# Kernel tuning notes

Measured on AMD Instinct MI355X. Metric: run time of the kernel, lower is better.

Reference implementation:

```python
import jax, jax.numpy as jnp
import numpy as np


def setup_inputs() -> dict:
    key = jax.random.key(0)
    ks = jax.random.split(key, 5)
    B, T, I, H = 32, 2048, 512, 512
    scale = 1.0 / np.sqrt(H)
    return {
        "x": jax.random.normal(ks[0], (B, T, I), dtype=jnp.float32),
        "h_0": jnp.zeros((B, H), dtype=jnp.float32),
        "Wx": jax.random.normal(ks[1], (H, I), dtype=jnp.float32) * scale,
        "bx": jax.random.normal(ks[2], (H,), dtype=jnp.float32) * scale,
        "Wh": jax.random.normal(ks[3], (H, H), dtype=jnp.float32) * scale,
        "bh": jax.random.normal(ks[4], (H,), dtype=jnp.float32) * scale,
    }


def reference(x, h_0, Wx, bx, Wh, bh):
    # Precompute input projection for all timesteps in one big GEMM: [B,T,H]
    x_proj = jnp.einsum("bti,hi->bth", x, Wx) + bx + bh

    def step(h, xp_t):  # h: [B,H], xp_t: [B,H]
        h_new = jnp.tanh(xp_t + h @ Wh.T)
        return h_new, h_new

    # scan over time axis: move T to leading dim
    h_last, outs = jax.lax.scan(step, h_0, jnp.swapaxes(x_proj, 0, 1))
    outputs = jnp.swapaxes(outs, 0, 1)  # [B,T,H]
    return outputs, h_last
```

## Files before the change

kernel.cpp:

```cpp
#include <hip/hip_runtime.h>


constexpr int Bb = 32, Tt = 2048, Ii = 512, Hh = 512;
constexpr int NP = 8;
constexpr int RP = Hh / NP;

static __device__ __forceinline__ float fast_tanh(float x) {
    float ax = fabsf(x);
    float e = __expf(-2.0f * ax);
    float r = (1.0f - e) / (1.0f + e);
    return copysignf(r, x);
}

__global__ __launch_bounds__(256, 2)
void xproj_gemm(const float* __restrict__ x, const float* __restrict__ Wx,
                const float* __restrict__ bx, const float* __restrict__ bh,
                float* __restrict__ xp)
{
    constexpr int BM = 128, BK = 16, LDT = BM + 4;
    __shared__ float As[BK][LDT];
    __shared__ float Bs[BK][LDT];

    const int tid = threadIdx.x;
    const int m0 = blockIdx.x * BM;
    const int n0 = blockIdx.y * BM;
    const int lrow = tid >> 1;
    const int lkh  = (tid & 1) * 8;
    const int tx = tid & 15, ty = tid >> 4;

    float acc[2][2][4][4] = {};

    for (int k0 = 0; k0 < Ii; k0 += BK) {
        float4 a0 = *reinterpret_cast<const float4*>(&x[(size_t)(m0 + lrow) * Ii + k0 + lkh]);
        float4 a1 = *reinterpret_cast<const float4*>(&x[(size_t)(m0 + lrow) * Ii + k0 + lkh + 4]);
        float4 b0 = *reinterpret_cast<const float4*>(&Wx[(size_t)(n0 + lrow) * Ii + k0 + lkh]);
        float4 b1 = *reinterpret_cast<const float4*>(&Wx[(size_t)(n0 + lrow) * Ii + k0 + lkh + 4]);
        __syncthreads();
        As[lkh + 0][lrow] = a0.x; As[lkh + 1][lrow] = a0.y;
        As[lkh + 2][lrow] = a0.z; As[lkh + 3][lrow] = a0.w;
        As[lkh + 4][lrow] = a1.x; As[lkh + 5][lrow] = a1.y;
        As[lkh + 6][lrow] = a1.z; As[lkh + 7][lrow] = a1.w;
        Bs[lkh + 0][lrow] = b0.x; Bs[lkh + 1][lrow] = b0.y;
        Bs[lkh + 2][lrow] = b0.z; Bs[lkh + 3][lrow] = b0.w;
        Bs[lkh + 4][lrow] = b1.x; Bs[lkh + 5][lrow] = b1.y;
        Bs[lkh + 6][lrow] = b1.z; Bs[lkh + 7][lrow] = b1.w;
        __syncthreads();
        #pragma unroll
        for (int k = 0; k < BK; ++k) {
            float4 av[2], bv[2];
            av[0] = *reinterpret_cast<const float4*>(&As[k][ty * 4]);
            av[1] = *reinterpret_cast<const float4*>(&As[k][64 + ty * 4]);
            bv[0] = *reinterpret_cast<const float4*>(&Bs[k][tx * 4]);
            bv[1] = *reinterpret_cast<const float4*>(&Bs[k][64 + tx * 4]);
            #pragma unroll
            for (int rh = 0; rh < 2; ++rh) {
                const float* ap = reinterpret_cast<const float*>(&av[rh]);
                #pragma unroll
                for (int ch = 0; ch < 2; ++ch) {
                    const float* bp = reinterpret_cast<const float*>(&bv[ch]);
                    #pragma unroll
                    for (int i = 0; i < 4; ++i)
                        #pragma unroll
                        for (int j = 0; j < 4; ++j)
                            acc[rh][ch][i][j] += ap[i] * bp[j];
                }
            }
        }
    }

    float4 bias[2];
    #pragma unroll
    for (int ch = 0; ch < 2; ++ch) {
        int cb = n0 + ch * 64 + tx * 4;
        bias[ch] = make_float4(bx[cb] + bh[cb], bx[cb + 1] + bh[cb + 1],
                               bx[cb + 2] + bh[cb + 2], bx[cb + 3] + bh[cb + 3]);
    }
    #pragma unroll
    for (int rh = 0; rh < 2; ++rh)
        #pragma unroll
        for (int i = 0; i < 4; ++i) {
            size_t row = (size_t)(m0 + rh * 64 + ty * 4 + i);
            #pragma unroll
            for (int ch = 0; ch < 2; ++ch) {
                const float* bp = reinterpret_cast<const float*>(&bias[ch]);
                float4 v = make_float4(acc[rh][ch][i][0] + bp[0], acc[rh][ch][i][1] + bp[1],
                                       acc[rh][ch][i][2] + bp[2], acc[rh][ch][i][3] + bp[3]);
                *reinterpret_cast<float4*>(&xp[row * Hh + n0 + ch * 64 + tx * 4]) = v;
            }
        }
}

__global__ void zero_xbuf(unsigned long long* __restrict__ xb)
{
    xb[(size_t)blockIdx.x * 512 + threadIdx.x] = 0ull;
}

__global__ __launch_bounds__(512, 1)
void rnn_scan_mb(const float* __restrict__ Wh, const float* __restrict__ h0,
                 float* __restrict__ out, unsigned long long* __restrict__ xbuf)
{
    const int bid = blockIdx.x;
    const int c = bid & 31;
    const int P = bid >> 5;
    const int tid = threadIdx.x;
    const int w = tid >> 6;
    const int lane = tid & 63;
    const int hf = lane >> 5, lp = lane & 31;
    const int lrow0 = w * 8 + hf * 4;

    __shared__ __align__(16) float hs[Hh];
    __shared__ __align__(16) float pacc[RP][36];

    float4 wreg[4][4];
    #pragma unroll
    for (int s = 0; s < 4; ++s)
        #pragma unroll
        for (int q = 0; q < 4; ++q) {
            const float* ap = &Wh[(size_t)(P * RP + lrow0 + s) * Hh + q * 128 + lp * 4];
            asm volatile("global_load_dwordx4 %0, %1, off"
                         : "=v"(wreg[s][q]) : "v"(ap));
        }
    asm volatile("s_waitcnt vmcnt(0)" ::: "memory");

    hs[tid] = h0[(size_t)c * Hh + tid];

    float* ob = out + (size_t)c * Tt * Hh;
    unsigned long long* xb = xbuf + (size_t)c * 2 * Hh;

    float xp_cur = 0.f;
    if (w == P) xp_cur = ob[P * RP + lane];
    __syncthreads();

    for (int t = 0; t < Tt; ++t) {
        float4 hv[4];
        #pragma unroll
        for (int q = 0; q < 4; ++q)
            hv[q] = *reinterpret_cast<const float4*>(&hs[q * 128 + lp * 4]);
        #pragma unroll
        for (int s = 0; s < 4; ++s) {
            float sum = 0.f;
            #pragma unroll
            for (int q = 0; q < 4; ++q) {
                const float* wq = reinterpret_cast<const float*>(&wreg[s][q]);
                const float* hq = reinterpret_cast<const float*>(&hv[q]);
                sum += wq[0] * hq[0]; sum += wq[1] * hq[1];
                sum += wq[2] * hq[2]; sum += wq[3] * hq[3];
            }
            pacc[lrow0 + s][lp] = sum;
        }
        __syncthreads();

        if (w == P) {
            float ssum = xp_cur;
            #pragma unroll
            for (int q = 0; q < 8; ++q) {
                float4 p4 = *reinterpret_cast<const float4*>(&pacc[lane][q * 4]);
                ssum += (p4.x + p4.y) + (p4.z + p4.w);
            }
            float hval = fast_tanh(ssum);
            ob[(size_t)t * Hh + P * RP + lane] = hval;
            if (t + 1 < Tt) {
                unsigned long long msg =
                    ((unsigned long long)(unsigned)(t + 1) << 32) |
                    (unsigned long long)__float_as_uint(hval);
                __hip_atomic_store(&xb[(size_t)(t & 1) * Hh + P * RP + lane], msg,
                                   __ATOMIC_RELAXED, __HIP_MEMORY_SCOPE_AGENT);
                hs[P * RP + lane] = hval;
                xp_cur = ob[(size_t)(t + 1) * Hh + P * RP + lane];
            } else {
                out[(size_t)Bb * Tt * Hh + (size_t)c * Hh + P * RP + lane] = hval;
            }
        } else if (t + 1 < Tt) {
            const unsigned want = (unsigned)(t + 1);
            unsigned long long msg;
            do {
                msg = __hip_atomic_load(&xb[(size_t)(t & 1) * Hh + w * RP + lane],
                                        __ATOMIC_RELAXED, __HIP_MEMORY_SCOPE_AGENT);
            } while ((unsigned)(msg >> 32) != want);
            hs[w * RP + lane] = __uint_as_float((unsigned)msg);
        }
        __syncthreads();
    }
}

__global__ __launch_bounds__(512)
void rnn_scan_sb(const float* __restrict__ W, const float* __restrict__ h0,
                 float* __restrict__ out)
{
    const int b = blockIdx.x;
    const int j = threadIdx.x;
    __shared__ float hsb[2][Hh];
    hsb[0][j] = h0[(size_t)b * Hh + j];
    __syncthreads();

    float* ob = out + (size_t)b * Tt * Hh;
    const float* wbase = W + (size_t)j * Hh;

    float xp_cur = ob[j];
    int cur = 0;
    for (int t = 0; t < Tt; ++t) {
        float xp_next = (t + 1 < Tt) ? ob[(size_t)(t + 1) * Hh + j] : 0.0f;
        float4 a = make_float4(xp_cur, 0.0f, 0.0f, 0.0f);
        const float* h = hsb[cur];
        #pragma unroll 8
        for (int c4 = 0; c4 < Hh / 4; ++c4) {
            float4 wv = *reinterpret_cast<const float4*>(&wbase[c4 * 4]);
            float4 hv = *reinterpret_cast<const float4*>(&h[c4 * 4]);
            a.x += wv.x * hv.x; a.y += wv.y * hv.y;
            a.z += wv.z * hv.z; a.w += wv.w * hv.w;
        }
        float hn = tanhf((a.x + a.y) + (a.z + a.w));
        hsb[cur ^ 1][j] = hn;
        ob[(size_t)t * Hh + j] = hn;
        xp_cur = xp_next;
        cur ^= 1;
        __syncthreads();
    }
    out[(size_t)Bb * Tt * Hh + (size_t)b * Hh + j] = hsb[cur][j];
}

extern "C" void kernel_launch(void* const* d_in, const int* in_sizes, int n_in,
                              void* d_out, int out_size, void* d_ws, size_t ws_size,
                              hipStream_t stream)
{
    const float* x  = (const float*)d_in[0];
    const float* h0 = (const float*)d_in[1];
    const float* Wx = (const float*)d_in[2];
    const float* bx = (const float*)d_in[3];
    const float* Wh = (const float*)d_in[4];
    const float* bh = (const float*)d_in[5];
    float* out = (float*)d_out;

    dim3 g1(Bb * Tt / 128, Hh / 128);
    xproj_gemm<<<g1, 256, 0, stream>>>(x, Wx, bx, bh, out);

    const size_t xb_bytes = (size_t)Bb * 2 * Hh * sizeof(unsigned long long);
    if (ws_size >= xb_bytes) {
        unsigned long long* xbuf = (unsigned long long*)d_ws;
        zero_xbuf<<<64, 512, 0, stream>>>(xbuf);
        void* args[] = {(void*)&Wh, (void*)&h0, (void*)&out, (void*)&xbuf};
        hipLaunchCooperativeKernel((void*)rnn_scan_mb, dim3(NP * Bb), dim3(512),
                                   args, 0, stream);
    } else {
        rnn_scan_sb<<<Bb, Hh, 0, stream>>>(Wh, h0, out);
    }
}
```

Baseline: 3.012 ms.

## Overlap cross-block flag polling with matvec and transpose partial-sum layout

Consumer warps now issue speculative atomic loads of the neighbour's hidden-state message while the per-step matvec is still running, and check them afterwards. This is meant to hide cross-block communication latency on the critical path of each timestep. The partial-sum buffer is transposed, so each lane writes one float4 and the finishing warp sums columns with four independent accumulators. The output store is moved after the atomic publish. The risk is extra memory traffic from the additional polling loads.

Result: slower. 3.821 ms (+26.9%).

```diff
diff --git a/kernel.cpp b/kernel.cpp
--- a/kernel.cpp
+++ b/kernel.cpp
@@ -109,7 +109,7 @@
     const int lrow0 = w * 8 + hf * 4;
 
     __shared__ __align__(16) float hs[Hh];
-    __shared__ __align__(16) float pacc[RP][36];
+    __shared__ __align__(16) float pq[32][68];
 
     float4 wreg[4][4];
     #pragma unroll
@@ -127,57 +127,108 @@
     float* ob = out + (size_t)c * Tt * Hh;
     unsigned long long* xb = xbuf + (size_t)c * 2 * Hh;
 
+    const bool isFin = (w == P);
     float xp_cur = 0.f;
-    if (w == P) xp_cur = ob[P * RP + lane];
+    if (isFin) xp_cur = ob[P * RP + lane];
     __syncthreads();
 
     for (int t = 0; t < Tt; ++t) {
-        float4 hv[4];
-        #pragma unroll
-        for (int q = 0; q < 4; ++q)
-            hv[q] = *reinterpret_cast<const float4*>(&hs[q * 128 + lp * 4]);
-        #pragma unroll
-        for (int s = 0; s < 4; ++s) {
-            float sum = 0.f;
-            #pragma unroll
-            for (int q = 0; q < 4; ++q) {
-                const float* wq = reinterpret_cast<const float*>(&wreg[s][q]);
-                const float* hq = reinterpret_cast<const float*>(&hv[q]);
-                sum += wq[0] * hq[0]; sum += wq[1] * hq[1];
-                sum += wq[2] * hq[2]; sum += wq[3] * hq[3];
-            }
-            pacc[lrow0 + s][lp] = sum;
-        }
-        __syncthreads();
-
-        if (w == P) {
-            float ssum = xp_cur;
-            #pragma unroll
-            for (int q = 0; q < 8; ++q) {
-                float4 p4 = *reinterpret_cast<const float4*>(&pacc[lane][q * 4]);
-                ssum += (p4.x + p4.y) + (p4.z + p4.w);
-            }
-            float hval = fast_tanh(ssum);
-            ob[(size_t)t * Hh + P * RP + lane] = hval;
+        const int d = t & 1;
+        const bool cons = (!isFin) && (t + 1 < Tt);
+        const unsigned long long* pa = &xb[(size_t)d * Hh + w * RP + lane];
+        unsigned long long mA = 0, mB = 0, mC = 0;
+
+        float4 hv0 = *reinterpret_cast<const float4*>(&hs[0 * 128 + lp * 4]);
+        float4 hv1 = *reinterpret_cast<const float4*>(&hs[1 * 128 + lp * 4]);
+        float4 hv2 = *reinterpret_cast<const float4*>(&hs[2 * 128 + lp * 4]);
+        float4 hv3 = *reinterpret_cast<const float4*>(&hs[3 * 128 + lp * 4]);
+
+        if (cons) mA = __hip_atomic_load(pa, __ATOMIC_RELAXED, __HIP_MEMORY_SCOPE_AGENT);
+        asm volatile("" ::: "memory");
+
+        float a0 = 0.f, a1 = 0.f, a2 = 0.f, a3 = 0.f;
+        {
+            const float* h0p = reinterpret_cast<const float*>(&hv0);
+            const float* h1p = reinterpret_cast<const float*>(&hv1);
+            #pragma unroll
+            for (int i = 0; i < 4; ++i) {
+                a0 += reinterpret_cast<const float*>(&wreg[0][0])[i] * h0p[i];
+                a1 += reinterpret_cast<const float*>(&wreg[1][0])[i] * h0p[i];
+                a2 += reinterpret_cast<const float*>(&wreg[2][0])[i] * h0p[i];
+                a3 += reinterpret_cast<const float*>(&wreg[3][0])[i] * h0p[i];
+            }
+            #pragma unroll
+            for (int i = 0; i < 4; ++i) {
+                a0 += reinterpret_cast<const float*>(&wreg[0][1])[i] * h1p[i];
+                a1 += reinterpret_cast<const float*>(&wreg[1][1])[i] * h1p[i];
+                a2 += reinterpret_cast<const float*>(&wreg[2][1])[i] * h1p[i];
+                a3 += reinterpret_cast<const float*>(&wreg[3][1])[i] * h1p[i];
+            }
+        }
+
+        if (cons) mB = __hip_atomic_load(pa, __ATOMIC_RELAXED, __HIP_MEMORY_SCOPE_AGENT);
+        asm volatile("" ::: "memory");
+
+        {
+            const float* h2p = reinterpret_cast<const float*>(&hv2);
+            const float* h3p = reinterpret_cast<const float*>(&hv3);
+            #pragma unroll
+            for (int i = 0; i < 4; ++i) {
+                a0 += reinterpret_cast<const float*>(&wreg[0][2])[i] * h2p[i];
+                a1 += reinterpret_cast<const float*>(&wreg[1][2])[i] * h2p[i];
+                a2 += reinterpret_cast<const float*>(&wreg[2][2])[i] * h2p[i];
+                a3 += reinterpret_cast<const float*>(&wreg[3][2])[i] * h2p[i];
+            }
+            #pragma unroll
+            for (int i = 0; i < 4; ++i) {
+                a0 += reinterpret_cast<const float*>(&wreg[0][3])[i] * h3p[i];
+                a1 += reinterpret_cast<const float*>(&wreg[1][3])[i] * h3p[i];
+                a2 += reinterpret_cast<const float*>(&wreg[2][3])[i] * h3p[i];
+                a3 += reinterpret_cast<const float*>(&wreg[3][3])[i] * h3p[i];
+            }
+        }
+
+        if (cons) mC = __hip_atomic_load(pa, __ATOMIC_RELAXED, __HIP_MEMORY_SCOPE_AGENT);
+        asm volatile("" ::: "memory");
+
+        *reinterpret_cast<float4*>(&pq[lp][lrow0]) = make_float4(a0, a1, a2, a3);
+        __syncthreads();
+
+        if (isFin) {
+            float s0 = xp_cur, s1 = 0.f, s2 = 0.f, s3 = 0.f;
+            #pragma unroll
+            for (int g = 0; g < 32; g += 4) {
+                s0 += pq[g + 0][lane];
+                s1 += pq[g + 1][lane];
+                s2 += pq[g + 2][lane];
+                s3 += pq[g + 3][lane];
+            }
+            float hval = fast_tanh((s0 + s1) + (s2 + s3));
             if (t + 1 < Tt) {
                 unsigned long long msg =
                     ((unsigned long long)(unsigned)(t + 1) << 32) |
                     (unsigned long long)__float_as_uint(hval);
-                __hip_atomic_store(&xb[(size_t)(t & 1) * Hh + P * RP + lane], msg,
+                __hip_atomic_store(&xb[(size_t)d * Hh + P * RP + lane], msg,
                                    __ATOMIC_RELAXED, __HIP_MEMORY_SCOPE_AGENT);
+                ob[(size_t)t * Hh + P * RP + lane] = hval;
                 hs[P * RP + lane] = hval;
                 xp_cur = ob[(size_t)(t + 1) * Hh + P * RP + lane];
             } else {
+                ob[(size_t)t * Hh + P * RP + lane] = hval;
                 out[(size_t)Bb * Tt * Hh + (size_t)c * Hh + P * RP + lane] = hval;
             }
-        } else if (t + 1 < Tt) {
+        } else if (cons) {
             const unsigned want = (unsigned)(t + 1);
-            unsigned long long msg;
-            do {
-                msg = __hip_atomic_load(&xb[(size_t)(t & 1) * Hh + w * RP + lane],
-                                        __ATOMIC_RELAXED, __HIP_MEMORY_SCOPE_AGENT);
-            } while ((unsigned)(msg >> 32) != want);
-            hs[w * RP + lane] = __uint_as_float((unsigned)msg);
+            unsigned val;
+            for (;;) {
+                if ((unsigned)(mA >> 32) == want) { val = (unsigned)mA; break; }
+                mA = __hip_atomic_load(pa, __ATOMIC_RELAXED, __HIP_MEMORY_SCOPE_AGENT);
+                if ((unsigned)(mB >> 32) == want) { val = (unsigned)mB; break; }
+                mB = __hip_atomic_load(pa, __ATOMIC_RELAXED, __HIP_MEMORY_SCOPE_AGENT);
+                if ((unsigned)(mC >> 32) == want) { val = (unsigned)mC; break; }
+                mC = __hip_atomic_load(pa, __ATOMIC_RELAXED, __HIP_MEMORY_SCOPE_AGENT);
+            }
+            hs[w * RP + lane] = __uint_as_float(val);
         }
         __syncthreads();
     }
```

## Transpose partial-sum buffer, move output store after publish, pipeline spin polling

Applied to the files above, without the earlier changes.

The shared partial-sum buffer is transposed to a padded [32][65] layout, so the finishing wave reduces with strided scalar reads spread over four independent accumulators. The global output store now comes after the atomic publish of the new hidden value, which takes it off the cross-block critical path. The spin-wait keeps three atomic loads in flight with short sleeps, aiming to cut the latency of seeing another block's update. The extra outstanding loads add memory traffic, and the scalar reduction issues more LDS instructions than the old float4 reads.

After: 3.881 ms. +28.8%, slower.

```diff
diff --git a/kernel.cpp b/kernel.cpp
--- a/kernel.cpp
+++ b/kernel.cpp
@@ -109,7 +109,7 @@
     const int lrow0 = w * 8 + hf * 4;
 
     __shared__ __align__(16) float hs[Hh];
-    __shared__ __align__(16) float pacc[RP][36];
+    __shared__ float pq[32][65];
 
     float4 wreg[4][4];
     #pragma unroll
@@ -127,15 +127,19 @@
     float* ob = out + (size_t)c * Tt * Hh;
     unsigned long long* xb = xbuf + (size_t)c * 2 * Hh;
 
+    const bool isFin = (w == P);
     float xp_cur = 0.f;
-    if (w == P) xp_cur = ob[P * RP + lane];
+    if (isFin) xp_cur = ob[P * RP + lane];
     __syncthreads();
 
     for (int t = 0; t < Tt; ++t) {
+        const int d = t & 1;
+
         float4 hv[4];
         #pragma unroll
         for (int q = 0; q < 4; ++q)
             hv[q] = *reinterpret_cast<const float4*>(&hs[q * 128 + lp * 4]);
+        float acc[4];
         #pragma unroll
         for (int s = 0; s < 4; ++s) {
             float sum = 0.f;
@@ -146,38 +150,55 @@
                 sum += wq[0] * hq[0]; sum += wq[1] * hq[1];
                 sum += wq[2] * hq[2]; sum += wq[3] * hq[3];
             }
-            pacc[lrow0 + s][lp] = sum;
-        }
-        __syncthreads();
-
-        if (w == P) {
-            float ssum = xp_cur;
-            #pragma unroll
-            for (int q = 0; q < 8; ++q) {
-                float4 p4 = *reinterpret_cast<const float4*>(&pacc[lane][q * 4]);
-                ssum += (p4.x + p4.y) + (p4.z + p4.w);
-            }
-            float hval = fast_tanh(ssum);
-            ob[(size_t)t * Hh + P * RP + lane] = hval;
+            acc[s] = sum;
+        }
+        #pragma unroll
+        for (int s = 0; s < 4; ++s)
+            pq[lp][lrow0 + s] = acc[s];
+        __syncthreads();
+
+        if (isFin) {
+            float s0 = xp_cur, s1 = 0.f, s2 = 0.f, s3 = 0.f;
+            #pragma unroll
+            for (int g = 0; g < 32; g += 4) {
+                s0 += pq[g + 0][lane];
+                s1 += pq[g + 1][lane];
+                s2 += pq[g + 2][lane];
+                s3 += pq[g + 3][lane];
+            }
+            float hval = fast_tanh((s0 + s1) + (s2 + s3));
             if (t + 1 < Tt) {
                 unsigned long long msg =
                     ((unsigned long long)(unsigned)(t + 1) << 32) |
                     (unsigned long long)__float_as_uint(hval);
-                __hip_atomic_store(&xb[(size_t)(t & 1) * Hh + P * RP + lane], msg,
+                __hip_atomic_store(&xb[(size_t)d * Hh + P * RP + lane], msg,
                                    __ATOMIC_RELAXED, __HIP_MEMORY_SCOPE_AGENT);
+                ob[(size_t)t * Hh + P * RP + lane] = hval;
                 hs[P * RP + lane] = hval;
                 xp_cur = ob[(size_t)(t + 1) * Hh + P * RP + lane];
             } else {
+                ob[(size_t)t * Hh + P * RP + lane] = hval;
                 out[(size_t)Bb * Tt * Hh + (size_t)c * Hh + P * RP + lane] = hval;
             }
         } else if (t + 1 < Tt) {
             const unsigned want = (unsigned)(t + 1);
-            unsigned long long msg;
-            do {
-                msg = __hip_atomic_load(&xb[(size_t)(t & 1) * Hh + w * RP + lane],
-                                        __ATOMIC_RELAXED, __HIP_MEMORY_SCOPE_AGENT);
-            } while ((unsigned)(msg >> 32) != want);
-            hs[w * RP + lane] = __uint_as_float((unsigned)msg);
+            const unsigned long long* pa = &xb[(size_t)d * Hh + w * RP + lane];
+            unsigned long long mA, mB, mC;
+            mA = __hip_atomic_load(pa, __ATOMIC_RELAXED, __HIP_MEMORY_SCOPE_AGENT);
+            __builtin_amdgcn_s_sleep(2);
+            mB = __hip_atomic_load(pa, __ATOMIC_RELAXED, __HIP_MEMORY_SCOPE_AGENT);
+            __builtin_amdgcn_s_sleep(2);
+            mC = __hip_atomic_load(pa, __ATOMIC_RELAXED, __HIP_MEMORY_SCOPE_AGENT);
+            unsigned val;
+            for (;;) {
+                if ((unsigned)(mA >> 32) == want) { val = (unsigned)mA; break; }
+                mA = __hip_atomic_load(pa, __ATOMIC_RELAXED, __HIP_MEMORY_SCOPE_AGENT);
+                if ((unsigned)(mB >> 32) == want) { val = (unsigned)mB; break; }
+                mB = __hip_atomic_load(pa, __ATOMIC_RELAXED, __HIP_MEMORY_SCOPE_AGENT);
+                if ((unsigned)(mC >> 32) == want) { val = (unsigned)mC; break; }
+                mC = __hip_atomic_load(pa, __ATOMIC_RELAXED, __HIP_MEMORY_SCOPE_AGENT);
+            }
+            hs[w * RP + lane] = __uint_as_float(val);
         }
         __syncthreads();
     }
```
